# Optimization experiments

Hardware: AMD Instinct MI355X
Metric: run time of the kernel (lower is better)

Reference implementation:

```python
import jax, jax.numpy as jnp
import numpy as np

NUM_CANDIDATES = 9
CENTER_IN_GT = True
MIN_IOU = 0.0
LEVELS = [262144, 32768, 4096, 512]  # anchors per FPN level (static)
NUM_GT = 64


def _to_box(c, s):
    lo = c - s / 2
    hi = c + s / 2
    # layout [x1, y1, x2, y2, z1, z2]
    return jnp.stack([lo[:, 0], lo[:, 1], hi[:, 0], hi[:, 1], lo[:, 2], hi[:, 2]], axis=1)


def setup_inputs() -> dict:
    key = jax.random.key(0)
    k1, k2, k3, k4 = jax.random.split(key, 4)
    n = sum(LEVELS)
    a_ctr = jax.random.uniform(k1, (n, 3), dtype=jnp.float32) * 512.0
    a_sz = jax.random.uniform(k2, (n, 3), dtype=jnp.float32) * 60.0 + 4.0
    g_ctr = jax.random.uniform(k3, (NUM_GT, 3), dtype=jnp.float32) * 512.0
    g_sz = jax.random.uniform(k4, (NUM_GT, 3), dtype=jnp.float32) * 90.0 + 10.0
    return {"gt_boxes": _to_box(g_ctr, g_sz), "anchors": _to_box(a_ctr, a_sz)}


def _centers(b):
    return jnp.stack([(b[:, 0] + b[:, 2]) / 2,
                      (b[:, 1] + b[:, 3]) / 2,
                      (b[:, 4] + b[:, 5]) / 2], axis=1)


def _iou(a, b):
    # a: (N,6), b: (M,6) -> (N,M) 3D IoU
    def vol(x):
        return (x[:, 2] - x[:, 0]) * (x[:, 3] - x[:, 1]) * (x[:, 5] - x[:, 4])
    v1, v2 = vol(a), vol(b)
    wx = jnp.clip(jnp.minimum(a[:, None, 2], b[None, :, 2]) - jnp.maximum(a[:, None, 0], b[None, :, 0]), 0.0)
    wy = jnp.clip(jnp.minimum(a[:, None, 3], b[None, :, 3]) - jnp.maximum(a[:, None, 1], b[None, :, 1]), 0.0)
    wz = jnp.clip(jnp.minimum(a[:, None, 5], b[None, :, 5]) - jnp.maximum(a[:, None, 4], b[None, :, 4]), 0.0)
    inter = wx * wy * wz
    return inter / (v1[:, None] + v2[None, :] - inter + 1e-6)


def reference(gt_boxes, anchors):
    n = anchors.shape[0]
    m = gt_boxes.shape[0]
    a_ctr = _centers(anchors)   # (N,3)
    g_ctr = _centers(gt_boxes)  # (M,3)

    # squared center distance (monotone in L2 distance, so topk ordering identical)
    d2 = ((a_ctr * a_ctr).sum(1)[:, None] + (g_ctr * g_ctr).sum(1)[None, :]
          - 2.0 * a_ctr @ g_ctr.T)  # (N,M)

    # per-level, per-GT top-k nearest anchors -> candidate set (vectorized over all GTs)
    cand_mask = jnp.zeros((n, m), dtype=bool)
    cand_idx_list = []
    gt_ids = jnp.arange(m)[:, None]
    start = 0
    for lvl in LEVELS:
        k = min(NUM_CANDIDATES, lvl)
        d_lvl = d2[start:start + lvl].T            # (M, lvl)
        _, idx = jax.lax.top_k(-d_lvl, k)          # smallest distances
        gidx = idx + start                         # (M, k) global anchor ids
        cand_mask = cand_mask.at[gidx, gt_ids].set(True)
        cand_idx_list.append(gidx)
        start += lvl
    cand_idx = jnp.concatenate(cand_idx_list, axis=1)  # (M, K_total)

    iou = _iou(anchors, gt_boxes)  # (N,M)

    # adaptive threshold per GT: mean + std (torch default: unbiased) over candidates
    cand_iou = jnp.take_along_axis(iou.T, cand_idx, axis=1)  # (M, K_total)
    thr = jnp.maximum(cand_iou.mean(axis=1) + cand_iou.std(axis=1, ddof=1), MIN_IOU)  # (M,)

    pos = cand_mask & (iou >= thr[None, :])
    if CENTER_IN_GT:
        inside = ((a_ctr[:, None, 0] >= gt_boxes[None, :, 0]) & (a_ctr[:, None, 0] <= gt_boxes[None, :, 2]) &
                  (a_ctr[:, None, 1] >= gt_boxes[None, :, 1]) & (a_ctr[:, None, 1] <= gt_boxes[None, :, 3]) &
                  (a_ctr[:, None, 2] >= gt_boxes[None, :, 4]) & (a_ctr[:, None, 2] <= gt_boxes[None, :, 5]))
        pos = pos & inside

    # conflict resolution: the sequential GT loop in the original assigns each anchor
    # to the positive GT with the highest IoU (ties -> earliest GT index) == argmax.
    any_pos = pos.any(axis=1)
    masked_iou = jnp.where(pos, iou, -jnp.inf)
    best = jnp.argmax(masked_iou, axis=1)  # (N,)
    matched_iou = jnp.where(any_pos, jnp.take_along_axis(iou, best[:, None], axis=1)[:, 0], 0.0)
    matched_gt_indices = jnp.where(any_pos, best, -1).astype(jnp.int32)
    labels = (matched_gt_indices >= 0).astype(jnp.int32)
    return matched_gt_indices, matched_iou, labels
```

## Files before the change

### kernel.cpp

```cpp
#include <hip/hip_runtime.h>
#include <cstdint>


#define NCAND 36
#define QCAP 64
#define OVF  0x80000000u
#define LVL1_START 262144
#define LVL2_START 294912
#define LVL2_MID   296960
#define LVL3_START 299008
#define SEG0 512
#define SEG1 64

__device__ __constant__ int   c_lvl_start[2] = {0, 262144};
__device__ __constant__ int   c_lvl_end[2]   = {262144, 294912};
__device__ __constant__ float c_T[2] = {961.0f, 3844.0f};

__device__ __forceinline__ unsigned f2ord(float f) {
    unsigned u = __float_as_uint(f);
    return (u & 0x80000000u) ? ~u : (u | 0x80000000u);
}

__device__ __forceinline__ void insertChain(unsigned long long e[9], unsigned long long x) {
    if (x < e[8]) {
        #pragma unroll
        for (int k = 0; k < 9; k++) {
            unsigned long long lo = (x < e[k]) ? x : e[k];
            unsigned long long hi = (x < e[k]) ? e[k] : x;
            e[k] = lo; x = hi;
        }
    }
}

__device__ __forceinline__ void waveTop9(unsigned long long e[9], int lane,
                                         unsigned long long* out9) {
    #pragma unroll
    for (int r9 = 0; r9 < 9; r9++) {
        unsigned long long mn = e[0];
        #pragma unroll
        for (int j = 1; j < 9; j++) mn = (e[j] < mn) ? e[j] : mn;
        #pragma unroll
        for (int off = 32; off >= 1; off >>= 1) {
            unsigned long long o = __shfl_xor(mn, off);
            mn = (o < mn) ? o : mn;
        }
        if (lane == 0) out9[r9] = mn;
        #pragma unroll
        for (int j = 0; j < 9; j++) e[j] = (e[j] == mn) ? ~0ULL : e[j];
    }
}

__device__ __forceinline__ void scanRange(const float* __restrict__ anchors,
                                          int s0, int s1, int lane,
                                          float gx, float gy, float gz, float sg,
                                          unsigned long long e[9]) {
    int i = s0 + lane;
    for (; i + 192 < s1; i += 256) {
        float2 q[4][3];
        #pragma unroll
        for (int u = 0; u < 4; u++) {
            const float2* r = (const float2*)(anchors + (size_t)(i + u*64)*6);
            q[u][0] = r[0]; q[u][1] = r[1]; q[u][2] = r[2];
        }
        #pragma unroll
        for (int u = 0; u < 4; u++) {
            float cx = (q[u][0].x + q[u][1].x) * 0.5f;
            float cy = (q[u][0].y + q[u][1].y) * 0.5f;
            float cz = (q[u][2].x + q[u][2].y) * 0.5f;
            float sa2 = cx*cx + cy*cy + cz*cz;
            float dot = cx*gx + cy*gy + cz*gz;
            float d2  = sa2 + sg - 2.0f*dot;
            insertChain(e, ((unsigned long long)f2ord(d2) << 32) | (unsigned)(i + u*64));
        }
    }
    for (; i < s1; i += 64) {
        const float2* r = (const float2*)(anchors + (size_t)i*6);
        float2 p0 = r[0], p1 = r[1], p2 = r[2];
        float cx = (p0.x + p1.x) * 0.5f;
        float cy = (p0.y + p1.y) * 0.5f;
        float cz = (p2.x + p2.y) * 0.5f;
        float sa2 = cx*cx + cy*cy + cz*cz;
        float dot = cx*gx + cy*gy + cz*gz;
        float d2  = sa2 + sg - 2.0f*dot;
        insertChain(e, ((unsigned long long)f2ord(d2) << 32) | (unsigned)i);
    }
}

__global__ void scanK(const float* __restrict__ anchors, const float* __restrict__ gt_boxes,
                      unsigned long long* __restrict__ l0, unsigned long long* __restrict__ l1,
                      unsigned* __restrict__ c0, unsigned* __restrict__ c1,
                      unsigned long long* __restrict__ packed, int n, int m) {
    int b    = blockIdx.x;
    int tid  = threadIdx.x;
    int base = b << 9;
    int lvl  = (base >= LVL1_START) ? 1 : 0;
    float T  = c_T[lvl];

    int segN = (lvl == 0) ? SEG0 : SEG1;
    int seg  = (lvl == 0) ? b : (b - SEG0);
    unsigned long long* lseg = (lvl == 0) ? l0 : l1;

    __shared__ float4 gt4[64];
    __shared__ unsigned qcnt[64];

    if (tid < 64) {
        qcnt[tid] = 0;
        if (tid < m) {
            int g = tid;
            float gx = (gt_boxes[g*6+0] + gt_boxes[g*6+2]) * 0.5f;
            float gy = (gt_boxes[g*6+1] + gt_boxes[g*6+3]) * 0.5f;
            float gz = (gt_boxes[g*6+4] + gt_boxes[g*6+5]) * 0.5f;
            float sg = gx*gx + gy*gy + gz*gz;
            gt4[g] = make_float4(gx, gy, gz, sg);
        }
    }
    if (b < 9) {
        int s = LVL2_START + (b << 9) + tid;
        if (s < n) packed[s] = 0ULL;
        if (s + 256 < n) packed[s + 256] = 0ULL;
    }
    __syncthreads();

    float ax[2], ay[2], az[2], sa[2];
    int   ai[2];
    #pragma unroll
    for (int k = 0; k < 2; k++) {
        int a = base + tid + k*256;
        ai[k] = a;
        const float2* r = (const float2*)(anchors + (size_t)a*6);
        float2 p0 = r[0], p1 = r[1], p2 = r[2];
        float cx = (p0.x + p1.x) * 0.5f;
        float cy = (p0.y + p1.y) * 0.5f;
        float cz = (p2.x + p2.y) * 0.5f;
        ax[k] = cx; ay[k] = cy; az[k] = cz;
        sa[k] = cx*cx + cy*cy + cz*cz;
        packed[a] = 0ULL;
    }

    for (int g = 0; g < m; g++) {
        float4 gv = gt4[g];
        size_t segoff = ((size_t)g * segN + seg) * QCAP;
        #pragma unroll
        for (int k = 0; k < 2; k++) {
            float dot = ax[k]*gv.x + ay[k]*gv.y + az[k]*gv.z;
            float d2  = sa[k] + gv.w - 2.0f*dot;
            if (d2 <= T) {
                unsigned idx = atomicAdd(&qcnt[g], 1u);
                if (idx < QCAP) {
                    unsigned long long p =
                        ((unsigned long long)f2ord(d2) << 32) | (unsigned)ai[k];
                    lseg[segoff + idx] = p;
                }
            }
        }
    }
    __syncthreads();

    if (tid < 64) {
        unsigned c = qcnt[tid];
        unsigned cw = (c > QCAP) ? OVF : c;
        if (lvl == 0) c0[tid * SEG0 + seg] = cw;
        else          c1[tid * SEG1 + seg] = cw;
    }
}

__global__ void selectC(const unsigned long long* __restrict__ l0,
                        const unsigned long long* __restrict__ l1,
                        const unsigned* __restrict__ c0,
                        const unsigned* __restrict__ c1,
                        const float* __restrict__ anchors,
                        const float* __restrict__ gt_boxes,
                        unsigned long long* __restrict__ packed, int n) {
    int g = blockIdx.x;
    int tid = threadIdx.x;
    int wl  = tid >> 6;
    int lane = tid & 63;
    __shared__ unsigned long long cands[NCAND];
    __shared__ unsigned long long cand2[18];

    float gx1 = gt_boxes[g*6+0], gy1 = gt_boxes[g*6+1];
    float gx2 = gt_boxes[g*6+2], gy2 = gt_boxes[g*6+3];
    float gz1 = gt_boxes[g*6+4], gz2 = gt_boxes[g*6+5];
    float gx = (gx1+gx2)*0.5f, gy = (gy1+gy2)*0.5f, gz = (gz1+gz2)*0.5f;
    float sg = gx*gx + gy*gy + gz*gz;

    unsigned long long e[9];
    #pragma unroll
    for (int k = 0; k < 9; k++) e[k] = ~0ULL;

    if (wl == 3) {
        scanRange(anchors, LVL3_START, n, lane, gx, gy, gz, sg, e);
        waveTop9(e, lane, &cands[27]);
        #pragma unroll
        for (int k = 0; k < 9; k++) e[k] = ~0ULL;
        scanRange(anchors, LVL2_MID, LVL3_START, lane, gx, gy, gz, sg, e);
        waveTop9(e, lane, &cand2[9]);
    } else if (wl == 2) {
        scanRange(anchors, LVL2_START, LVL2_MID, lane, gx, gy, gz, sg, e);
        waveTop9(e, lane, &cand2[0]);
    } else {
        int segN = (wl == 0) ? SEG0 : SEG1;
        int J    = (wl == 0) ? 8 : 1;
        const unsigned* cc = (wl == 0) ? c0 : c1;
        const unsigned long long* ll = (wl == 0) ? l0 : l1;
        size_t sb = (size_t)g * segN * QCAP;

        unsigned cs[8];
        unsigned long long q0[8];
        unsigned tot = 0, ovf = 0;
        #pragma unroll
        for (int j = 0; j < 8; j++) {
            cs[j] = 0; q0[j] = ~0ULL;
            if (j < J) {
                cs[j] = cc[(size_t)g * segN + lane + 64*j];
                q0[j] = ll[sb + (size_t)(lane + 64*j) * QCAP];
            }
        }
        #pragma unroll
        for (int j = 0; j < 8; j++) {
            if (j < J) { if (cs[j] & OVF) ovf = 1; else tot += cs[j]; }
        }
        #pragma unroll
        for (int o = 32; o >= 1; o >>= 1) {
            tot += __shfl_xor(tot, o);
            ovf |= __shfl_xor(ovf, o);
        }

        if (!ovf && tot >= 9) {
            #pragma unroll
            for (int j = 0; j < 8; j++) {
                if (j < J) {
                    unsigned c = cs[j];
                    if (c >= 1) insertChain(e, q0[j]);
                    size_t segoff = sb + (size_t)(lane + 64*j) * QCAP;
                    for (unsigned s = 1; s < c; s++)
                        insertChain(e, ll[segoff + s]);
                }
            }
        } else {
            scanRange(anchors, c_lvl_start[wl], c_lvl_end[wl], lane, gx, gy, gz, sg, e);
        }
        waveTop9(e, lane, &cands[wl*9]);
    }
    __syncthreads();

    if (wl == 2) {
        unsigned long long v = (lane < 18) ? cand2[lane] : ~0ULL;
        #pragma unroll
        for (int r9 = 0; r9 < 9; r9++) {
            unsigned long long mn = v;
            #pragma unroll
            for (int off = 32; off >= 1; off >>= 1) {
                unsigned long long o = __shfl_xor(mn, off);
                mn = (o < mn) ? o : mn;
            }
            if (lane == 0) cands[18 + r9] = mn;
            v = (v == mn) ? ~0ULL : v;
        }
    }
    __syncthreads();

    if (tid < 64) {
        float vg = (gx2 - gx1) * (gy2 - gy1) * (gz2 - gz1);
        bool valid = (tid < NCAND);
        float iou = 0.0f;
        int aidx = 0;
        float acx = 0.0f, acy = 0.0f, acz = 0.0f;
        if (valid) {
            aidx = (int)(unsigned)cands[tid];
            float ax1 = anchors[aidx*6+0], ay1 = anchors[aidx*6+1];
            float ax2 = anchors[aidx*6+2], ay2 = anchors[aidx*6+3];
            float az1 = anchors[aidx*6+4], az2 = anchors[aidx*6+5];
            float va = (ax2 - ax1) * (ay2 - ay1) * (az2 - az1);
            float wx = fmaxf(fminf(ax2, gx2) - fmaxf(ax1, gx1), 0.0f);
            float wy = fmaxf(fminf(ay2, gy2) - fmaxf(ay1, gy1), 0.0f);
            float wz = fmaxf(fminf(az2, gz2) - fmaxf(az1, gz1), 0.0f);
            float inter = wx * wy * wz;
            iou = inter / (va + vg - inter + 1e-6f);
            acx = (ax1 + ax2) * 0.5f;
            acy = (ay1 + ay2) * 0.5f;
            acz = (az1 + az2) * 0.5f;
        }

        float s = iou;
        #pragma unroll
        for (int o = 32; o >= 1; o >>= 1) s += __shfl_xor(s, o);
        float mean = s / 36.0f;
        float dev = valid ? (iou - mean) : 0.0f;
        float s2 = dev * dev;
        #pragma unroll
        for (int o = 32; o >= 1; o >>= 1) s2 += __shfl_xor(s2, o);
        float thr = fmaxf(mean + sqrtf(s2 / 35.0f), 0.0f);

        if (valid && iou >= thr) {
            bool inside = (acx >= gx1) & (acx <= gx2) &
                          (acy >= gy1) & (acy <= gy2) &
                          (acz >= gz1) & (acz <= gz2);
            if (inside) {
                unsigned long long p =
                    ((unsigned long long)__float_as_uint(iou) << 32) | (unsigned)(~(unsigned)g);
                atomicMax(&packed[aidx], p);
            }
        }
    }
}

__global__ void phaseD(const unsigned long long* __restrict__ packed,
                       float* __restrict__ out, int n) {
    int i = blockIdx.x * blockDim.x + threadIdx.x;
    if (i >= n) return;
    unsigned long long p = packed[i];
    float gt_f, iou_f, lab_f;
    if (p == 0ULL) {
        gt_f = -1.0f; iou_f = 0.0f; lab_f = 0.0f;
    } else {
        unsigned low = (unsigned)p;
        int gidx = (int)(~low);
        iou_f = __uint_as_float((unsigned)(p >> 32));
        gt_f = (float)gidx;
        lab_f = 1.0f;
    }
    out[i]       = gt_f;
    out[n + i]   = iou_f;
    out[2*n + i] = lab_f;
}

extern "C" void kernel_launch(void* const* d_in, const int* in_sizes, int n_in,
                              void* d_out, int out_size, void* d_ws, size_t ws_size,
                              hipStream_t stream) {
    const float* gt      = (const float*)d_in[0];
    const float* anchors = (const float*)d_in[1];
    int m = in_sizes[0] / 6;
    int n = in_sizes[1] / 6;

    char* ws = (char*)d_ws;
    unsigned long long* packed = (unsigned long long*)ws;
    size_t off = (size_t)n * 8;
    unsigned long long* l0 = (unsigned long long*)(ws + off);
    off += (size_t)64 * SEG0 * QCAP * 8;
    unsigned long long* l1 = (unsigned long long*)(ws + off);
    off += (size_t)64 * SEG1 * QCAP * 8;
    unsigned* c0 = (unsigned*)(ws + off);
    off += (size_t)64 * SEG0 * 4;
    unsigned* c1 = (unsigned*)(ws + off);
    float* out = (float*)d_out;

    scanK<<<SEG0 + SEG1, 256, 0, stream>>>(anchors, gt, l0, l1, c0, c1, packed, n, m);
    selectC<<<m, 256, 0, stream>>>(l0, l1, c0, c1, anchors, gt, packed, n);
    phaseD<<<(n + 255) / 256, 256, 0, stream>>>(packed, out, n);
}
```

Baseline: 46.62 us.

## Precompute level-2/3 anchor centers into float4 buffer and vectorize candidate-list loads

```diff
diff --git a/kernel.cpp b/kernel.cpp
--- a/kernel.cpp
+++ b/kernel.cpp
@@ -7,10 +7,10 @@
 #define OVF  0x80000000u
 #define LVL1_START 262144
 #define LVL2_START 294912
-#define LVL2_MID   296960
 #define LVL3_START 299008
 #define SEG0 512
 #define SEG1 64
+#define C4BLOCKS 9
 
 __device__ __constant__ int   c_lvl_start[2] = {0, 262144};
 __device__ __constant__ int   c_lvl_end[2]   = {262144, 294912};
@@ -47,6 +47,32 @@
         if (lane == 0) out9[r9] = mn;
         #pragma unroll
         for (int j = 0; j < 9; j++) e[j] = (e[j] == mn) ? ~0ULL : e[j];
+    }
+}
+
+__device__ __forceinline__ void scanC4(const float4* __restrict__ c4,
+                                       int rel0, int rel1, int lane,
+                                       float gx, float gy, float gz, float sg,
+                                       unsigned long long e[9]) {
+    int i = rel0 + lane;
+    for (; i + 448 < rel1; i += 512) {
+        float4 q[8];
+        #pragma unroll
+        for (int u = 0; u < 8; u++) q[u] = c4[i + u*64];
+        #pragma unroll
+        for (int u = 0; u < 8; u++) {
+            float dot = q[u].x*gx + q[u].y*gy + q[u].z*gz;
+            float d2  = q[u].w + sg - 2.0f*dot;
+            insertChain(e, ((unsigned long long)f2ord(d2) << 32)
+                           | (unsigned)(LVL2_START + i + u*64));
+        }
+    }
+    for (; i < rel1; i += 64) {
+        float4 q = c4[i];
+        float dot = q.x*gx + q.y*gy + q.z*gz;
+        float d2  = q.w + sg - 2.0f*dot;
+        insertChain(e, ((unsigned long long)f2ord(d2) << 32)
+                       | (unsigned)(LVL2_START + i));
     }
 }
 
@@ -89,9 +115,30 @@
 __global__ void scanK(const float* __restrict__ anchors, const float* __restrict__ gt_boxes,
                       unsigned long long* __restrict__ l0, unsigned long long* __restrict__ l1,
                       unsigned* __restrict__ c0, unsigned* __restrict__ c1,
-                      unsigned long long* __restrict__ packed, int n, int m) {
+                      unsigned long long* __restrict__ packed,
+                      float4* __restrict__ c4, int n, int m) {
     int b    = blockIdx.x;
     int tid  = threadIdx.x;
+
+    if (b >= SEG0 + SEG1) {
+        int bb = b - (SEG0 + SEG1);
+        int i0 = LVL2_START + (bb << 9) + tid;
+        #pragma unroll
+        for (int k = 0; k < 2; k++) {
+            int i = i0 + k*256;
+            if (i < n) {
+                const float2* r = (const float2*)(anchors + (size_t)i*6);
+                float2 p0 = r[0], p1 = r[1], p2 = r[2];
+                float cx = (p0.x + p1.x) * 0.5f;
+                float cy = (p0.y + p1.y) * 0.5f;
+                float cz = (p2.x + p2.y) * 0.5f;
+                float sa2 = cx*cx + cy*cy + cz*cz;
+                c4[i - LVL2_START] = make_float4(cx, cy, cz, sa2);
+            }
+        }
+        return;
+    }
+
     int base = b << 9;
     int lvl  = (base >= LVL1_START) ? 1 : 0;
     float T  = c_T[lvl];
@@ -170,6 +217,7 @@
                         const unsigned* __restrict__ c1,
                         const float* __restrict__ anchors,
                         const float* __restrict__ gt_boxes,
+                        const float4* __restrict__ c4,
                         unsigned long long* __restrict__ packed, int n) {
     int g = blockIdx.x;
     int tid = threadIdx.x;
@@ -189,37 +237,26 @@
     for (int k = 0; k < 9; k++) e[k] = ~0ULL;
 
     if (wl == 3) {
-        scanRange(anchors, LVL3_START, n, lane, gx, gy, gz, sg, e);
+        scanC4(c4, LVL3_START - LVL2_START, n - LVL2_START, lane, gx, gy, gz, sg, e);
         waveTop9(e, lane, &cands[27]);
         #pragma unroll
         for (int k = 0; k < 9; k++) e[k] = ~0ULL;
-        scanRange(anchors, LVL2_MID, LVL3_START, lane, gx, gy, gz, sg, e);
+        scanC4(c4, 2048, LVL3_START - LVL2_START, lane, gx, gy, gz, sg, e);
         waveTop9(e, lane, &cand2[9]);
     } else if (wl == 2) {
-        scanRange(anchors, LVL2_START, LVL2_MID, lane, gx, gy, gz, sg, e);
+        scanC4(c4, 0, 2048, lane, gx, gy, gz, sg, e);
         waveTop9(e, lane, &cand2[0]);
-    } else {
-        int segN = (wl == 0) ? SEG0 : SEG1;
-        int J    = (wl == 0) ? 8 : 1;
-        const unsigned* cc = (wl == 0) ? c0 : c1;
-        const unsigned long long* ll = (wl == 0) ? l0 : l1;
-        size_t sb = (size_t)g * segN * QCAP;
-
-        unsigned cs[8];
-        unsigned long long q0[8];
-        unsigned tot = 0, ovf = 0;
-        #pragma unroll
-        for (int j = 0; j < 8; j++) {
-            cs[j] = 0; q0[j] = ~0ULL;
-            if (j < J) {
-                cs[j] = cc[(size_t)g * segN + lane + 64*j];
-                q0[j] = ll[sb + (size_t)(lane + 64*j) * QCAP];
-            }
-        }
-        #pragma unroll
-        for (int j = 0; j < 8; j++) {
-            if (j < J) { if (cs[j] & OVF) ovf = 1; else tot += cs[j]; }
-        }
+    } else if (wl == 1) {
+        size_t sb = (size_t)g * SEG1 * QCAP;
+        unsigned c = c1[(size_t)g * SEG1 + lane];
+        size_t so = sb + (size_t)lane * QCAP;
+        ulonglong2 q01 = *(const ulonglong2*)(l1 + so);
+        ulonglong2 q23 = *(const ulonglong2*)(l1 + so + 2);
+        ulonglong2 q45 = *(const ulonglong2*)(l1 + so + 4);
+        ulonglong2 q67 = *(const ulonglong2*)(l1 + so + 6);
+
+        unsigned ovf = (c & OVF) ? 1u : 0u;
+        unsigned tot = ovf ? 0u : c;
         #pragma unroll
         for (int o = 32; o >= 1; o >>= 1) {
             tot += __shfl_xor(tot, o);
@@ -227,20 +264,63 @@
         }
 
         if (!ovf && tot >= 9) {
+            if (c >= 1) insertChain(e, q01.x);
+            if (c >= 2) insertChain(e, q01.y);
+            if (c >= 3) insertChain(e, q23.x);
+            if (c >= 4) insertChain(e, q23.y);
+            if (c >= 5) insertChain(e, q45.x);
+            if (c >= 6) insertChain(e, q45.y);
+            if (c >= 7) insertChain(e, q67.x);
+            if (c >= 8) insertChain(e, q67.y);
+            for (unsigned s = 8; s < c; s++)
+                insertChain(e, l1[so + s]);
+        } else {
+            scanRange(anchors, c_lvl_start[1], c_lvl_end[1], lane, gx, gy, gz, sg, e);
+        }
+        waveTop9(e, lane, &cands[9]);
+    } else {
+        size_t sb = (size_t)g * SEG0 * QCAP;
+        unsigned cs[8];
+        ulonglong2 p01[8], p23[8];
+        #pragma unroll
+        for (int j = 0; j < 8; j++)
+            cs[j] = c0[(size_t)g * SEG0 + lane + 64*j];
+        #pragma unroll
+        for (int j = 0; j < 8; j++) {
+            size_t so = sb + (size_t)(lane + 64*j) * QCAP;
+            p01[j] = *(const ulonglong2*)(l0 + so);
+            p23[j] = *(const ulonglong2*)(l0 + so + 2);
+        }
+
+        unsigned tot = 0, ovf = 0;
+        #pragma unroll
+        for (int j = 0; j < 8; j++) {
+            if (cs[j] & OVF) ovf = 1; else tot += cs[j];
+        }
+        #pragma unroll
+        for (int o = 32; o >= 1; o >>= 1) {
+            tot += __shfl_xor(tot, o);
+            ovf |= __shfl_xor(ovf, o);
+        }
+
+        if (!ovf && tot >= 9) {
             #pragma unroll
             for (int j = 0; j < 8; j++) {
-                if (j < J) {
-                    unsigned c = cs[j];
-                    if (c >= 1) insertChain(e, q0[j]);
-                    size_t segoff = sb + (size_t)(lane + 64*j) * QCAP;
-                    for (unsigned s = 1; s < c; s++)
-                        insertChain(e, ll[segoff + s]);
+                unsigned c = cs[j];
+                if (c >= 1) insertChain(e, p01[j].x);
+                if (c >= 2) insertChain(e, p01[j].y);
+                if (c >= 3) insertChain(e, p23[j].x);
+                if (c >= 4) insertChain(e, p23[j].y);
+                if (c > 4) {
+                    size_t so = sb + (size_t)(lane + 64*j) * QCAP;
+                    for (unsigned s = 4; s < c; s++)
+                        insertChain(e, l0[so + s]);
                 }
             }
         } else {
-            scanRange(anchors, c_lvl_start[wl], c_lvl_end[wl], lane, gx, gy, gz, sg, e);
-        }
-        waveTop9(e, lane, &cands[wl*9]);
+            scanRange(anchors, c_lvl_start[0], c_lvl_end[0], lane, gx, gy, gz, sg, e);
+        }
+        waveTop9(e, lane, &cands[0]);
     }
     __syncthreads();
 
@@ -343,9 +423,12 @@
     unsigned* c0 = (unsigned*)(ws + off);
     off += (size_t)64 * SEG0 * 4;
     unsigned* c1 = (unsigned*)(ws + off);
+    off += (size_t)64 * SEG1 * 4;
+    float4* c4 = (float4*)(ws + off);
     float* out = (float*)d_out;
 
-    scanK<<<SEG0 + SEG1, 256, 0, stream>>>(anchors, gt, l0, l1, c0, c1, packed, n, m);
-    selectC<<<m, 256, 0, stream>>>(l0, l1, c0, c1, anchors, gt, packed, n);
+    scanK<<<SEG0 + SEG1 + C4BLOCKS, 256, 0, stream>>>(anchors, gt, l0, l1, c0, c1,
+                                                      packed, c4, n, m);
+    selectC<<<m, 256, 0, stream>>>(l0, l1, c0, c1, anchors, gt, c4, packed, n);
     phaseD<<<(n + 255) / 256, 256, 0, stream>>>(packed, out, n);
 }
```

Measured after the change: 45.76 us. No clear change (-1.8%).
